# Performance work log

Measured on AMD Instinct MI355X. Metric: run time of the kernel, lower is better.

## Reference

```python
import jax, jax.numpy as jnp
import numpy as np

B, S, D, H, L, V, P = 4, 1024, 768, 12, 6, 50257, 1024
Dh = D // H
DF = 4 * D
LN_EPS = 1e-5


def _ln(x, g, b):
    mu = jnp.mean(x, axis=-1, keepdims=True)
    var = jnp.mean(jnp.square(x - mu), axis=-1, keepdims=True)
    return (x - mu) * jax.lax.rsqrt(var + LN_EPS) * g + b


def setup_inputs() -> dict:
    key = jax.random.key(0)
    ks = jax.random.split(key, 12)
    init = lambda k, shape: (jax.random.normal(k, shape, jnp.float32) * 0.02)
    inp = {
        'input_ids': jax.random.randint(ks[0], (B, S), 0, V).astype(jnp.int32),
        'remaining_frames_ids': jax.random.randint(ks[1], (B, S), 0, V).astype(jnp.int32),
        'wte': init(ks[2], (V, D)),
        'wte_rf': init(ks[3], (V, D)),
        'wpe': init(ks[4], (P, D)),
        'ln1_g': jnp.ones((L, D), jnp.float32), 'ln1_b': jnp.zeros((L, D), jnp.float32),
        'attn_w': init(ks[5], (L, D, 3 * D)), 'attn_b': jnp.zeros((L, 3 * D), jnp.float32),
        'proj_w': init(ks[6], (L, D, D)), 'proj_b': jnp.zeros((L, D), jnp.float32),
        'ln2_g': jnp.ones((L, D), jnp.float32), 'ln2_b': jnp.zeros((L, D), jnp.float32),
        'fc_w': init(ks[7], (L, D, DF)), 'fc_b': jnp.zeros((L, DF), jnp.float32),
        'fc2_w': init(ks[8], (L, DF, D)), 'fc2_b': jnp.zeros((L, D), jnp.float32),
        'lnf_g': jnp.ones((D,), jnp.float32), 'lnf_b': jnp.zeros((D,), jnp.float32),
    }
    return inp


def _block(h, lg1, lb1, aw, ab, pw, pb, lg2, lb2, fw, fb, f2w, f2b, causal):
    a = _ln(h, lg1, lb1)
    qkv = jnp.einsum('bsd,de->bse', a, aw) + ab          # [B,S,3D]
    q, k, v = jnp.split(qkv, 3, axis=-1)
    split = lambda t: t.reshape(B, S, H, Dh).transpose(0, 2, 1, 3)  # [B,H,S,Dh]
    q, k, v = split(q), split(k), split(v)
    w = jnp.einsum('bhqd,bhkd->bhqk', q, k) / jnp.sqrt(jnp.asarray(Dh, q.dtype))
    w = w * causal - 10000.0 * (1.0 - causal)
    w = jax.nn.softmax(w, axis=-1)
    o = jnp.einsum('bhqk,bhkd->bhqd', w, v)
    o = o.transpose(0, 2, 1, 3).reshape(B, S, D)
    o = jnp.einsum('bsd,de->bse', o, pw) + pb
    h = h + o
    m = _ln(h, lg2, lb2)
    m = jax.nn.gelu(jnp.einsum('bsd,df->bsf', m, fw) + fb, approximate=True)
    m = jnp.einsum('bsf,fd->bsd', m, f2w) + f2b
    return h + m


def reference(input_ids, remaining_frames_ids, wte, wte_rf, wpe,
              ln1_g, ln1_b, attn_w, attn_b, proj_w, proj_b,
              ln2_g, ln2_b, fc_w, fc_b, fc2_w, fc2_b, lnf_g, lnf_b):
    h = wte[input_ids] + wte_rf[remaining_frames_ids] + wpe[:S][None, :, :]
    i = jnp.arange(S)[:, None]
    j = jnp.arange(S)[None, :]
    causal = (i >= j).astype(h.dtype)[None, None, :, :]   # nd == ns
    for l in range(L):
        h = _block(h, ln1_g[l], ln1_b[l], attn_w[l], attn_b[l], proj_w[l], proj_b[l],
                   ln2_g[l], ln2_b[l], fc_w[l], fc_b[l], fc2_w[l], fc2_b[l], causal)
    return _ln(h, lnf_g, lnf_b)
```

## Files before the change

kernel.cpp:

```cpp
#include <hip/hip_runtime.h>
#include <hip/hip_bf16.h>
#include <math.h>

#define BB 4
#define SS 1024
#define DD 768
#define HH 12
#define NLAYER 6
#define DHH 64
#define DFF 3072
#define D3 2304
#define LN_EPS 1e-5f

typedef __hip_bfloat16 bf16;
typedef short bf16x8 __attribute__((ext_vector_type(8)));
typedef float f32x4 __attribute__((ext_vector_type(4)));

__device__ __forceinline__ void gload_lds16(const void* g, void* l) {
  __builtin_amdgcn_global_load_lds(
      (const __attribute__((address_space(1))) void*)g,
      (__attribute__((address_space(3))) void*)l, 16, 0, 0);
}

__device__ __forceinline__ unsigned short f2bf_bits(float x) {
  bf16 h = __float2bfloat16(x);
  union { bf16 h; unsigned short u; } c; c.h = h; return c.u;
}

__global__ __launch_bounds__(256) void embed_kernel(
    const int* __restrict__ ids, const int* __restrict__ rf,
    const float* __restrict__ wte, const float* __restrict__ wte_rf,
    const float* __restrict__ wpe, float* __restrict__ h)
{
  int idx = blockIdx.x * 256 + threadIdx.x;
  int token = idx / (DD / 4);
  int c4 = (idx % (DD / 4)) * 4;
  int s = token % SS;
  int id  = ids[token];
  int rid = rf[token];
  float4 a = *(const float4*)(wte    + (size_t)id  * DD + c4);
  float4 b = *(const float4*)(wte_rf + (size_t)rid * DD + c4);
  float4 c = *(const float4*)(wpe    + (size_t)s   * DD + c4);
  float4 o;
  o.x = a.x + b.x + c.x;
  o.y = a.y + b.y + c.y;
  o.z = a.z + b.z + c.z;
  o.w = a.w + b.w + c.w;
  *(float4*)(h + (size_t)token * DD + c4) = o;
}

__global__ __launch_bounds__(256) void transpose_cast(
    const float* __restrict__ W, bf16* __restrict__ Wt, int K, int N)
{
  __shared__ float tile[32][33];
  int n0 = blockIdx.x * 32, k0 = blockIdx.y * 32;
  int tx = threadIdx.x & 31, ty = threadIdx.x >> 5;
  #pragma unroll
  for (int i = 0; i < 4; ++i)
    tile[ty + 8 * i][tx] = W[(size_t)(k0 + ty + 8 * i) * N + n0 + tx];
  __syncthreads();
  #pragma unroll
  for (int i = 0; i < 4; ++i)
    Wt[(size_t)(n0 + ty + 8 * i) * K + k0 + tx] = __float2bfloat16(tile[tx][ty + 8 * i]);
}

__global__ __launch_bounds__(256) void vtrans_kernel(
    const bf16* __restrict__ qkv, bf16* __restrict__ vt)
{
  __shared__ unsigned short tile[32][34];
  int bh = blockIdx.z, b = bh / HH, h = bh % HH;
  int s0 = blockIdx.x * 32, d0 = blockIdx.y * 32;
  int tx = threadIdx.x & 31, ty = threadIdx.x >> 5;
  const unsigned short* src =
      (const unsigned short*)qkv + (size_t)b * SS * D3 + 2 * DD + h * DHH;
  #pragma unroll
  for (int i = 0; i < 4; ++i)
    tile[ty + 8 * i][tx] = src[(size_t)(s0 + ty + 8 * i) * D3 + d0 + tx];
  __syncthreads();
  unsigned short* dst = (unsigned short*)vt + (size_t)bh * DHH * SS;
  #pragma unroll
  for (int i = 0; i < 4; ++i)
    dst[(size_t)(d0 + ty + 8 * i) * SS + s0 + tx] = tile[tx][ty + 8 * i];
}

template <typename OutT>
__global__ __launch_bounds__(192) void ln_kernel(
    const float* __restrict__ x, const float* __restrict__ g,
    const float* __restrict__ bb, OutT* __restrict__ y)
{
  __shared__ float red[2][3];
  int row = blockIdx.x;
  int t = threadIdx.x;
  const float* xr = x + (size_t)row * DD;
  float4 v = *(const float4*)(xr + t * 4);
  float s  = v.x + v.y + v.z + v.w;
  float sq = v.x * v.x + v.y * v.y + v.z * v.z + v.w * v.w;
  #pragma unroll
  for (int off = 32; off > 0; off >>= 1) {
    s  += __shfl_down(s, off);
    sq += __shfl_down(sq, off);
  }
  int wave = t >> 6, lane = t & 63;
  if (lane == 0) { red[0][wave] = s; red[1][wave] = sq; }
  __syncthreads();
  s  = red[0][0] + red[0][1] + red[0][2];
  sq = red[1][0] + red[1][1] + red[1][2];
  float mu   = s * (1.0f / DD);
  float var  = sq * (1.0f / DD) - mu * mu;
  float rstd = rsqrtf(var + LN_EPS);
  float4 gv = *(const float4*)(g  + t * 4);
  float4 bv = *(const float4*)(bb + t * 4);
  float o0 = (v.x - mu) * rstd * gv.x + bv.x;
  float o1 = (v.y - mu) * rstd * gv.y + bv.y;
  float o2 = (v.z - mu) * rstd * gv.z + bv.z;
  float o3 = (v.w - mu) * rstd * gv.w + bv.w;
  if constexpr (sizeof(OutT) == 4) {
    float4 o = {o0, o1, o2, o3};
    *(float4*)((float*)y + (size_t)row * DD + t * 4) = o;
  } else {
    ushort4 o = {f2bf_bits(o0), f2bf_bits(o1), f2bf_bits(o2), f2bf_bits(o3)};
    *(ushort4*)((unsigned short*)y + (size_t)row * DD + t * 4) = o;
  }
}

__device__ __forceinline__ float gelu_f(float x) {
  float x3 = x * x * x;
  return 0.5f * x * (1.0f + tanhf(0.7978845608028654f * (x + 0.044715f * x3)));
}

template <int BM, int BN, int WM, int WN, int MODE, typename OutT>
__global__ __launch_bounds__(256) void gemm_bf16(
    const bf16* __restrict__ A,
    const bf16* __restrict__ Wt,
    const float* __restrict__ bias,
    const float* __restrict__ R,
    OutT* __restrict__ C, int M, int N, int K)
{
  constexpr int MR = WM / 16, NR = WN / 16;
  constexpr int WC = BN / WN;
  constexpr int ACH = BM * 4 / 256, BCH = BN * 4 / 256;
  constexpr int ABUF = BM * 64, BBUF = BN * 64;
  static_assert((BM / WM) * (BN / WN) == 4, "4 waves");
  __shared__ alignas(16) char AsB[2 * ABUF];
  __shared__ alignas(16) char BsB[2 * BBUF];
  const int t = threadIdx.x;
  const int lane = t & 63, wid = t >> 6;
  const int wr = wid / WC, wc = wid % WC;
  const int g = lane >> 4, l15 = lane & 15;

  const int nx = gridDim.x;
  const int nwg = nx * gridDim.y;
  const int bid0 = blockIdx.y * nx + blockIdx.x;
  const int bid = (bid0 & 7) * (nwg >> 3) + (bid0 >> 3);
  const int bm = (bid / nx) * BM, bn = (bid % nx) * BN;

  f32x4 acc[MR][NR] = {};

  const unsigned short* Ag[ACH];
  const unsigned short* Bg[BCH];
  #pragma unroll
  for (int i = 0; i < ACH; ++i) {
    int c = t + i * 256;
    Ag[i] = (const unsigned short*)A + (size_t)(bm + c % BM) * K + (c / BM) * 8;
  }
  #pragma unroll
  for (int i = 0; i < BCH; ++i) {
    int c = t + i * 256;
    Bg[i] = (const unsigned short*)Wt + (size_t)(bn + c % BN) * K + (c / BN) * 8;
  }

  auto stage = [&](int buf, int k0) {
    #pragma unroll
    for (int i = 0; i < ACH; ++i)
      gload_lds16(Ag[i] + k0, AsB + buf * ABUF + (t + i * 256) * 16);
    #pragma unroll
    for (int i = 0; i < BCH; ++i)
      gload_lds16(Bg[i] + k0, BsB + buf * BBUF + (t + i * 256) * 16);
  };

  const int abase = g * (BM * 16) + (wr * WM + l15) * 16;
  const int bbase = g * (BN * 16) + (wc * WN + l15) * 16;

  const int nt = K / 32;
  stage(0, 0);
  __syncthreads();
  for (int tk = 0; tk < nt; ++tk) {
    const int cur = tk & 1;
    if (tk + 1 < nt) stage(cur ^ 1, (tk + 1) * 32);
    bf16x8 a[MR], b[NR];
    #pragma unroll
    for (int m = 0; m < MR; ++m)
      a[m] = *(const bf16x8*)(AsB + cur * ABUF + abase + m * 256);
    #pragma unroll
    for (int n = 0; n < NR; ++n)
      b[n] = *(const bf16x8*)(BsB + cur * BBUF + bbase + n * 256);
    #pragma unroll
    for (int m = 0; m < MR; ++m)
      #pragma unroll
      for (int n = 0; n < NR; ++n)
        acc[m][n] = __builtin_amdgcn_mfma_f32_16x16x32_bf16(a[m], b[n], acc[m][n], 0, 0, 0);
    __syncthreads();
  }

  const int colg = l15, rowg = g * 4;
  #pragma unroll
  for (int m = 0; m < MR; ++m) {
    #pragma unroll
    for (int n = 0; n < NR; ++n) {
      int col = bn + wc * WN + n * 16 + colg;
      float bv = bias[col];
      #pragma unroll
      for (int r = 0; r < 4; ++r) {
        int row = bm + wr * WM + m * 16 + rowg + r;
        float v = acc[m][n][r] + bv;
        if constexpr (MODE == 1) v += R[(size_t)row * N + col];
        if constexpr (MODE == 2) v = gelu_f(v);
        if constexpr (sizeof(OutT) == 4) ((float*)C)[(size_t)row * N + col] = v;
        else ((bf16*)C)[(size_t)row * N + col] = __float2bfloat16(v);
      }
    }
  }
}

__global__ __launch_bounds__(256) void attn_mfma(
    const bf16* __restrict__ qkv,
    const bf16* __restrict__ vt,
    bf16* __restrict__ o)
{
  __shared__ unsigned short plds[4][16][40];
  const int bid = blockIdx.x;
  const int swz = (bid & 7) * 96 + (bid >> 3);
  const int bh = swz >> 4, qt = swz & 15;
  const int b = bh / HH, h = bh % HH;
  const int w = threadIdx.x >> 6, lane = threadIdx.x & 63;
  const int g = lane >> 4, l15 = lane & 15;
  const int q0 = qt * 64 + w * 16;
  const int qg = q0 + l15;

  const bf16* qbase = qkv + (size_t)b * SS * D3 + h * DHH;
  const bf16* kbase = qbase + DD;
  const bf16* vbase = vt + (size_t)bh * DHH * SS;

  bf16x8 qf0 = *(const bf16x8*)(qbase + (size_t)(q0 + l15) * D3 + g * 8);
  bf16x8 qf1 = *(const bf16x8*)(qbase + (size_t)(q0 + l15) * D3 + 32 + g * 8);

  f32x4 oacc[4] = {};
  float m = -1e30f, l = 0.f;
  const int kvend = q0 + 16;

  for (int kv0 = 0; kv0 < kvend; kv0 += 32) {
    f32x4 st[2];
    #pragma unroll
    for (int tt = 0; tt < 2; ++tt) {
      const bf16* kr = kbase + (size_t)(kv0 + tt * 16 + l15) * D3 + g * 8;
      bf16x8 kf0 = *(const bf16x8*)kr;
      bf16x8 kf1 = *(const bf16x8*)(kr + 32);
      f32x4 z = {0.f, 0.f, 0.f, 0.f};
      z = __builtin_amdgcn_mfma_f32_16x16x32_bf16(kf0, qf0, z, 0, 0, 0);
      z = __builtin_amdgcn_mfma_f32_16x16x32_bf16(kf1, qf1, z, 0, 0, 0);
      st[tt] = z;
    }
    float sv[8];
    #pragma unroll
    for (int tt = 0; tt < 2; ++tt)
      #pragma unroll
      for (int r = 0; r < 4; ++r) {
        int kv = kv0 + tt * 16 + 4 * g + r;
        float x = st[tt][r] * 0.125f;
        sv[tt * 4 + r] = (kv > qg) ? -1e30f : x;
      }
    float pmax = sv[0];
    #pragma unroll
    for (int i = 1; i < 8; ++i) pmax = fmaxf(pmax, sv[i]);
    pmax = fmaxf(pmax, __shfl_xor(pmax, 16));
    pmax = fmaxf(pmax, __shfl_xor(pmax, 32));
    float mnew = fmaxf(m, pmax);
    float alpha = __expf(m - mnew);
    float rsum = 0.f;
    ushort4 pA, pB;
    {
      float p0 = __expf(sv[0] - mnew), p1 = __expf(sv[1] - mnew);
      float p2 = __expf(sv[2] - mnew), p3 = __expf(sv[3] - mnew);
      float p4 = __expf(sv[4] - mnew), p5 = __expf(sv[5] - mnew);
      float p6 = __expf(sv[6] - mnew), p7 = __expf(sv[7] - mnew);
      rsum = ((p0 + p1) + (p2 + p3)) + ((p4 + p5) + (p6 + p7));
      pA.x = f2bf_bits(p0); pA.y = f2bf_bits(p1); pA.z = f2bf_bits(p2); pA.w = f2bf_bits(p3);
      pB.x = f2bf_bits(p4); pB.y = f2bf_bits(p5); pB.z = f2bf_bits(p6); pB.w = f2bf_bits(p7);
    }
    rsum += __shfl_xor(rsum, 16);
    rsum += __shfl_xor(rsum, 32);
    l = l * alpha + rsum; m = mnew;
    #pragma unroll
    for (int blk = 0; blk < 4; ++blk)
      #pragma unroll
      for (int r = 0; r < 4; ++r) oacc[blk][r] *= alpha;

    *(ushort4*)&plds[w][l15][4 * g]      = pA;
    *(ushort4*)&plds[w][l15][16 + 4 * g] = pB;
    asm volatile("s_waitcnt lgkmcnt(0)" ::: "memory");
    __builtin_amdgcn_sched_barrier(0);

    bf16x8 pf = *(const bf16x8*)&plds[w][l15][g * 8];
    #pragma unroll
    for (int blk = 0; blk < 4; ++blk) {
      bf16x8 vf = *(const bf16x8*)(vbase + (size_t)(blk * 16 + l15) * SS + kv0 + g * 8);
      oacc[blk] = __builtin_amdgcn_mfma_f32_16x16x32_bf16(vf, pf, oacc[blk], 0, 0, 0);
    }
  }

  float linv = 1.0f / l;
  unsigned short* ob = (unsigned short*)o + (size_t)(b * SS + qg) * DD + h * DHH;
  #pragma unroll
  for (int blk = 0; blk < 4; ++blk) {
    ushort4 ov = {f2bf_bits(oacc[blk][0] * linv), f2bf_bits(oacc[blk][1] * linv),
                  f2bf_bits(oacc[blk][2] * linv), f2bf_bits(oacc[blk][3] * linv)};
    *(ushort4*)(ob + blk * 16 + 4 * g) = ov;
  }
}

extern "C" void kernel_launch(void* const* d_in, const int* in_sizes, int n_in,
                              void* d_out, int out_size, void* d_ws, size_t ws_size,
                              hipStream_t stream)
{
  (void)in_sizes; (void)n_in; (void)out_size; (void)ws_size;
  const int*   ids    = (const int*)d_in[0];
  const int*   rfids  = (const int*)d_in[1];
  const float* wte    = (const float*)d_in[2];
  const float* wte_rf = (const float*)d_in[3];
  const float* wpe    = (const float*)d_in[4];
  const float* ln1_g  = (const float*)d_in[5];
  const float* ln1_b  = (const float*)d_in[6];
  const float* attn_w = (const float*)d_in[7];
  const float* attn_b = (const float*)d_in[8];
  const float* proj_w = (const float*)d_in[9];
  const float* proj_b = (const float*)d_in[10];
  const float* ln2_g  = (const float*)d_in[11];
  const float* ln2_b  = (const float*)d_in[12];
  const float* fc_w   = (const float*)d_in[13];
  const float* fc_b   = (const float*)d_in[14];
  const float* fc2_w  = (const float*)d_in[15];
  const float* fc2_b  = (const float*)d_in[16];
  const float* lnf_g  = (const float*)d_in[17];
  const float* lnf_b  = (const float*)d_in[18];

  const int T = BB * SS;
  const size_t TD = (size_t)T * DD;
  float* h    = (float*)d_ws;
  bf16*  qkvb = (bf16*)(h + TD);
  bf16*  vtb  = qkvb + (size_t)T * D3;
  bf16*  ff   = qkvb;
  bf16*  a    = vtb + TD;
  bf16*  att  = a;
  bf16*  awt  = a + TD;
  bf16*  pwt  = awt + (size_t)D3 * DD;
  bf16*  fwt  = pwt + (size_t)DD * DD;
  bf16*  f2wt = fwt + (size_t)DFF * DD;

  embed_kernel<<<dim3((T * DD / 4) / 256), 256, 0, stream>>>(ids, rfids, wte, wte_rf, wpe, h);

  for (int l = 0; l < NLAYER; ++l) {
    transpose_cast<<<dim3(D3 / 32,  DD / 32),  256, 0, stream>>>(attn_w + (size_t)l * DD * D3,  awt,  DD,  D3);
    transpose_cast<<<dim3(DD / 32,  DD / 32),  256, 0, stream>>>(proj_w + (size_t)l * DD * DD,  pwt,  DD,  DD);
    transpose_cast<<<dim3(DFF / 32, DD / 32),  256, 0, stream>>>(fc_w   + (size_t)l * DD * DFF, fwt,  DD,  DFF);
    transpose_cast<<<dim3(DD / 32,  DFF / 32), 256, 0, stream>>>(fc2_w  + (size_t)l * DFF * DD, f2wt, DFF, DD);

    ln_kernel<bf16><<<T, 192, 0, stream>>>(h, ln1_g + (size_t)l * DD, ln1_b + (size_t)l * DD, a);
    gemm_bf16<128, 128, 64, 64, 0, bf16><<<dim3(D3 / 128, T / 128), 256, 0, stream>>>(
        a, awt, attn_b + (size_t)l * D3, nullptr, qkvb, T, D3, DD);
    vtrans_kernel<<<dim3(SS / 32, DHH / 32, BB * HH), 256, 0, stream>>>(qkvb, vtb);
    attn_mfma<<<BB * HH * (SS / 64), 256, 0, stream>>>(qkvb, vtb, att);
    gemm_bf16<64, 128, 32, 64, 1, float><<<dim3(DD / 128, T / 64), 256, 0, stream>>>(
        att, pwt, proj_b + (size_t)l * DD, h, h, T, DD, DD);
    ln_kernel<bf16><<<T, 192, 0, stream>>>(h, ln2_g + (size_t)l * DD, ln2_b + (size_t)l * DD, a);
    gemm_bf16<128, 128, 64, 64, 2, bf16><<<dim3(DFF / 128, T / 128), 256, 0, stream>>>(
        a, fwt, fc_b + (size_t)l * DFF, nullptr, ff, T, DFF, DD);
    gemm_bf16<64, 128, 32, 64, 1, float><<<dim3(DD / 128, T / 64), 256, 0, stream>>>(
        ff, f2wt, fc2_b + (size_t)l * DD, h, h, T, DD, DFF);
  }
  ln_kernel<float><<<T, 192, 0, stream>>>(h, lnf_g, lnf_b, (float*)d_out);
}
```

Measured before the change: 2.191 ms.

## Pair causal query tiles per block and software-prefetch K/V in attention

Each attention block now processes two 64-row query tiles (p and 15-p), so every block does about the same amount of causal work, and the grid is halved. Inside each strip, the K and V fragments for the next kv tile are loaded from global memory while the current tile's MFMAs and softmax run, hiding load latency. MFMA sections are also wrapped in s_setprio. The risks are higher register pressure from the prefetched fragments and half as many blocks to fill the CUs.

```diff
diff --git a/kernel.cpp b/kernel.cpp
--- a/kernel.cpp
+++ b/kernel.cpp
@@ -222,53 +222,52 @@
   }
 }
 
-__global__ __launch_bounds__(256) void attn_mfma(
-    const bf16* __restrict__ qkv,
-    const bf16* __restrict__ vt,
-    bf16* __restrict__ o)
-{
-  __shared__ unsigned short plds[4][16][40];
-  const int bid = blockIdx.x;
-  const int swz = (bid & 7) * 96 + (bid >> 3);
-  const int bh = swz >> 4, qt = swz & 15;
-  const int b = bh / HH, h = bh % HH;
-  const int w = threadIdx.x >> 6, lane = threadIdx.x & 63;
-  const int g = lane >> 4, l15 = lane & 15;
-  const int q0 = qt * 64 + w * 16;
+__device__ __forceinline__ void attn_strip(
+    const bf16* __restrict__ qbase, const bf16* __restrict__ kbase,
+    const bf16* __restrict__ vbase, unsigned short (*pw)[40],
+    bf16* __restrict__ o, int b, int h, int q0, int g, int l15)
+{
   const int qg = q0 + l15;
-
-  const bf16* qbase = qkv + (size_t)b * SS * D3 + h * DHH;
-  const bf16* kbase = qbase + DD;
-  const bf16* vbase = vt + (size_t)bh * DHH * SS;
-
-  bf16x8 qf0 = *(const bf16x8*)(qbase + (size_t)(q0 + l15) * D3 + g * 8);
-  bf16x8 qf1 = *(const bf16x8*)(qbase + (size_t)(q0 + l15) * D3 + 32 + g * 8);
-
-  f32x4 oacc[4] = {};
+  const int kvend = q0 + 16;
+  bf16x8 qf0 = *(const bf16x8*)(qbase + (size_t)qg * D3 + g * 8);
+  bf16x8 qf1 = *(const bf16x8*)(qbase + (size_t)qg * D3 + 32 + g * 8);
+  f32x4 oa0 = {}, oa1 = {}, oa2 = {}, oa3 = {};
   float m = -1e30f, l = 0.f;
-  const int kvend = q0 + 16;
+
+  const bf16* kr = kbase + (size_t)l15 * D3 + g * 8;
+  bf16x8 k00 = *(const bf16x8*)(kr);
+  bf16x8 k01 = *(const bf16x8*)(kr + 32);
+  bf16x8 k10 = *(const bf16x8*)(kr + (size_t)16 * D3);
+  bf16x8 k11 = *(const bf16x8*)(kr + (size_t)16 * D3 + 32);
+  const bf16* vr = vbase + (size_t)l15 * SS + g * 8;
+  bf16x8 v0 = *(const bf16x8*)(vr);
+  bf16x8 v1 = *(const bf16x8*)(vr + (size_t)16 * SS);
+  bf16x8 v2 = *(const bf16x8*)(vr + (size_t)32 * SS);
+  bf16x8 v3 = *(const bf16x8*)(vr + (size_t)48 * SS);
 
   for (int kv0 = 0; kv0 < kvend; kv0 += 32) {
-    f32x4 st[2];
-    #pragma unroll
-    for (int tt = 0; tt < 2; ++tt) {
-      const bf16* kr = kbase + (size_t)(kv0 + tt * 16 + l15) * D3 + g * 8;
-      bf16x8 kf0 = *(const bf16x8*)kr;
-      bf16x8 kf1 = *(const bf16x8*)(kr + 32);
-      f32x4 z = {0.f, 0.f, 0.f, 0.f};
-      z = __builtin_amdgcn_mfma_f32_16x16x32_bf16(kf0, qf0, z, 0, 0, 0);
-      z = __builtin_amdgcn_mfma_f32_16x16x32_bf16(kf1, qf1, z, 0, 0, 0);
-      st[tt] = z;
+    f32x4 s0 = {0.f, 0.f, 0.f, 0.f}, s1 = {0.f, 0.f, 0.f, 0.f};
+    __builtin_amdgcn_s_setprio(1);
+    s0 = __builtin_amdgcn_mfma_f32_16x16x32_bf16(k00, qf0, s0, 0, 0, 0);
+    s0 = __builtin_amdgcn_mfma_f32_16x16x32_bf16(k01, qf1, s0, 0, 0, 0);
+    s1 = __builtin_amdgcn_mfma_f32_16x16x32_bf16(k10, qf0, s1, 0, 0, 0);
+    s1 = __builtin_amdgcn_mfma_f32_16x16x32_bf16(k11, qf1, s1, 0, 0, 0);
+    __builtin_amdgcn_s_setprio(0);
+
+    const int kvn = (kv0 + 32 < kvend) ? kv0 + 32 : 0;
+    const bf16* krn = kbase + (size_t)(kvn + l15) * D3 + g * 8;
+    bf16x8 nk00 = *(const bf16x8*)(krn);
+    bf16x8 nk01 = *(const bf16x8*)(krn + 32);
+    bf16x8 nk10 = *(const bf16x8*)(krn + (size_t)16 * D3);
+    bf16x8 nk11 = *(const bf16x8*)(krn + (size_t)16 * D3 + 32);
+
+    float sv[8];
+    #pragma unroll
+    for (int r = 0; r < 4; ++r) {
+      int kva = kv0 + 4 * g + r, kvb = kv0 + 16 + 4 * g + r;
+      sv[r]     = (kva > qg) ? -1e30f : s0[r] * 0.125f;
+      sv[4 + r] = (kvb > qg) ? -1e30f : s1[r] * 0.125f;
     }
-    float sv[8];
-    #pragma unroll
-    for (int tt = 0; tt < 2; ++tt)
-      #pragma unroll
-      for (int r = 0; r < 4; ++r) {
-        int kv = kv0 + tt * 16 + 4 * g + r;
-        float x = st[tt][r] * 0.125f;
-        sv[tt * 4 + r] = (kv > qg) ? -1e30f : x;
-      }
     float pmax = sv[0];
     #pragma unroll
     for (int i = 1; i < 8; ++i) pmax = fmaxf(pmax, sv[i]);
@@ -276,7 +275,7 @@
     pmax = fmaxf(pmax, __shfl_xor(pmax, 32));
     float mnew = fmaxf(m, pmax);
     float alpha = __expf(m - mnew);
-    float rsum = 0.f;
+    float rsum;
     ushort4 pA, pB;
     {
       float p0 = __expf(sv[0] - mnew), p1 = __expf(sv[1] - mnew);
@@ -291,31 +290,66 @@
     rsum += __shfl_xor(rsum, 32);
     l = l * alpha + rsum; m = mnew;
     #pragma unroll
-    for (int blk = 0; blk < 4; ++blk)
-      #pragma unroll
-      for (int r = 0; r < 4; ++r) oacc[blk][r] *= alpha;
-
-    *(ushort4*)&plds[w][l15][4 * g]      = pA;
-    *(ushort4*)&plds[w][l15][16 + 4 * g] = pB;
+    for (int r = 0; r < 4; ++r) {
+      oa0[r] *= alpha; oa1[r] *= alpha; oa2[r] *= alpha; oa3[r] *= alpha;
+    }
+
+    *(ushort4*)&pw[l15][4 * g]      = pA;
+    *(ushort4*)&pw[l15][16 + 4 * g] = pB;
     asm volatile("s_waitcnt lgkmcnt(0)" ::: "memory");
     __builtin_amdgcn_sched_barrier(0);
-
-    bf16x8 pf = *(const bf16x8*)&plds[w][l15][g * 8];
-    #pragma unroll
-    for (int blk = 0; blk < 4; ++blk) {
-      bf16x8 vf = *(const bf16x8*)(vbase + (size_t)(blk * 16 + l15) * SS + kv0 + g * 8);
-      oacc[blk] = __builtin_amdgcn_mfma_f32_16x16x32_bf16(vf, pf, oacc[blk], 0, 0, 0);
-    }
+    bf16x8 pf = *(const bf16x8*)&pw[l15][g * 8];
+
+    __builtin_amdgcn_s_setprio(1);
+    oa0 = __builtin_amdgcn_mfma_f32_16x16x32_bf16(v0, pf, oa0, 0, 0, 0);
+    oa1 = __builtin_amdgcn_mfma_f32_16x16x32_bf16(v1, pf, oa1, 0, 0, 0);
+    oa2 = __builtin_amdgcn_mfma_f32_16x16x32_bf16(v2, pf, oa2, 0, 0, 0);
+    oa3 = __builtin_amdgcn_mfma_f32_16x16x32_bf16(v3, pf, oa3, 0, 0, 0);
+    __builtin_amdgcn_s_setprio(0);
+
+    const bf16* vrn = vbase + (size_t)l15 * SS + kvn + g * 8;
+    v0 = *(const bf16x8*)(vrn);
+    v1 = *(const bf16x8*)(vrn + (size_t)16 * SS);
+    v2 = *(const bf16x8*)(vrn + (size_t)32 * SS);
+    v3 = *(const bf16x8*)(vrn + (size_t)48 * SS);
+    k00 = nk00; k01 = nk01; k10 = nk10; k11 = nk11;
   }
 
   float linv = 1.0f / l;
   unsigned short* ob = (unsigned short*)o + (size_t)(b * SS + qg) * DD + h * DHH;
-  #pragma unroll
-  for (int blk = 0; blk < 4; ++blk) {
-    ushort4 ov = {f2bf_bits(oacc[blk][0] * linv), f2bf_bits(oacc[blk][1] * linv),
-                  f2bf_bits(oacc[blk][2] * linv), f2bf_bits(oacc[blk][3] * linv)};
-    *(ushort4*)(ob + blk * 16 + 4 * g) = ov;
-  }
+  ushort4 w0 = {f2bf_bits(oa0[0] * linv), f2bf_bits(oa0[1] * linv),
+                f2bf_bits(oa0[2] * linv), f2bf_bits(oa0[3] * linv)};
+  ushort4 w1 = {f2bf_bits(oa1[0] * linv), f2bf_bits(oa1[1] * linv),
+                f2bf_bits(oa1[2] * linv), f2bf_bits(oa1[3] * linv)};
+  ushort4 w2 = {f2bf_bits(oa2[0] * linv), f2bf_bits(oa2[1] * linv),
+                f2bf_bits(oa2[2] * linv), f2bf_bits(oa2[3] * linv)};
+  ushort4 w3 = {f2bf_bits(oa3[0] * linv), f2bf_bits(oa3[1] * linv),
+                f2bf_bits(oa3[2] * linv), f2bf_bits(oa3[3] * linv)};
+  *(ushort4*)(ob + 0 * 16 + 4 * g) = w0;
+  *(ushort4*)(ob + 1 * 16 + 4 * g) = w1;
+  *(ushort4*)(ob + 2 * 16 + 4 * g) = w2;
+  *(ushort4*)(ob + 3 * 16 + 4 * g) = w3;
+}
+
+__global__ __launch_bounds__(256) void attn_mfma(
+    const bf16* __restrict__ qkv,
+    const bf16* __restrict__ vt,
+    bf16* __restrict__ o)
+{
+  __shared__ unsigned short plds[4][16][40];
+  const int bid = blockIdx.x;
+  const int swz = (bid & 7) * 48 + (bid >> 3);
+  const int bh = swz >> 3, p = swz & 7;
+  const int b = bh / HH, h = bh % HH;
+  const int w = threadIdx.x >> 6, lane = threadIdx.x & 63;
+  const int g = lane >> 4, l15 = lane & 15;
+
+  const bf16* qbase = qkv + (size_t)b * SS * D3 + h * DHH;
+  const bf16* kbase = qbase + DD;
+  const bf16* vbase = vt + (size_t)bh * DHH * SS;
+
+  attn_strip(qbase, kbase, vbase, plds[w], o, b, h, p * 64 + w * 16, g, l15);
+  attn_strip(qbase, kbase, vbase, plds[w], o, b, h, (15 - p) * 64 + w * 16, g, l15);
 }
 
 extern "C" void kernel_launch(void* const* d_in, const int* in_sizes, int n_in,
@@ -368,7 +402,7 @@
     gemm_bf16<128, 128, 64, 64, 0, bf16><<<dim3(D3 / 128, T / 128), 256, 0, stream>>>(
         a, awt, attn_b + (size_t)l * D3, nullptr, qkvb, T, D3, DD);
     vtrans_kernel<<<dim3(SS / 32, DHH / 32, BB * HH), 256, 0, stream>>>(qkvb, vtb);
-    attn_mfma<<<BB * HH * (SS / 64), 256, 0, stream>>>(qkvb, vtb, att);
+    attn_mfma<<<BB * HH * (SS / 64) / 2, 256, 0, stream>>>(qkvb, vtb, att);
     gemm_bf16<64, 128, 32, 64, 1, float><<<dim3(DD / 128, T / 64), 256, 0, stream>>>(
         att, pwt, proj_b + (size_t)l * DD, h, h, T, DD, DD);
     ln_kernel<bf16><<<T, 192, 0, stream>>>(h, ln2_g + (size_t)l * DD, ln2_b + (size_t)l * DD, a);
```

Measured after the change: 2.058 ms. 6.1% less time.
